# Performance work log

Measured on AMD Instinct MI355X. Metric: run time of the kernel, lower is better.

Reference implementation:

```python
import jax, jax.numpy as jnp
import numpy as np

B, T, D = 4, 1024, 1024
H = 16
DH = D // H  # 64
NEG = jnp.float32(-2.0**32 + 1)


def _sinusoid_table(T, D):
    pos = np.arange(T)[:, None]
    i = np.arange(D)[None, :]
    angle = pos / np.power(10000.0, 2.0 * (i // 2) / D)
    tab = np.zeros((T, D))
    tab[:, 0::2] = np.sin(angle[:, 0::2])
    tab[:, 1::2] = np.cos(angle[:, 1::2])
    return jnp.asarray(tab, dtype=jnp.float32)


def setup_inputs() -> dict:
    key = jax.random.key(0)
    ks = jax.random.split(key, 10)
    inp = {
        "queries": jax.random.normal(ks[0], (B, T, D), dtype=jnp.float32),
        "keys": jax.random.normal(ks[1], (B, T, D), dtype=jnp.float32),
        "query_lens": jax.random.randint(ks[2], (B, 1), 1, T + 1),
        "key_lens": jax.random.randint(ks[3], (B, 1), 1, T + 1),
        # learned params
        "pe_q": _sinusoid_table(T, D),
        "pe_k": _sinusoid_table(T, D),
        "W_Query": jax.random.truncated_normal(ks[4], -2.0, 2.0, (D, D), dtype=jnp.float32) * 0.05,
        "W_key": jax.random.truncated_normal(ks[5], -2.0, 2.0, (D, D), dtype=jnp.float32) * 0.05,
        "W_Value": jax.random.truncated_normal(ks[6], -2.0, 2.0, (D, D), dtype=jnp.float32) * 0.05,
        "fw1": jax.random.normal(ks[7], (D, 4 * D), dtype=jnp.float32) * (1.0 / np.sqrt(D)),
        "fw2": jax.random.normal(ks[8], (4 * D, D), dtype=jnp.float32) * (1.0 / np.sqrt(4 * D)),
    }
    return inp


def _forward(queries, keys, pe_q, pe_k, W_Query, W_key, W_Value, fw1, fw2,
             query_lens, key_lens):
    scale = jnp.float32(np.sqrt(D))
    # positional encoding (scale=True). NOTE: source bug preserved —
    # keys tensor is overwritten by key_pe applied to the PE'd queries.
    q_in = queries + pe_q[None] * scale          # [B,T,D]
    k_in = q_in + pe_k[None] * scale             # [B,T,D]

    Q = q_in @ W_Query                           # [B,T,D]
    K = k_in @ W_key                             # [B,T,D]
    V = K @ W_Value                              # NOTE: V projected from projected keys (source quirk)

    def heads(x):  # [B,T,D] -> [H,B,T,DH]
        return x.reshape(B, T, H, DH).transpose(2, 0, 1, 3)

    Qh, Kh, Vh = heads(Q), heads(K), heads(V)
    scores = jnp.einsum("hbqd,hbkd->hbqk", Qh, Kh) / jnp.float32(np.sqrt(DH))

    t = jnp.arange(T)
    kmask = (t[None, :] < key_lens).astype(jnp.float32)    # [B,T]
    qmask = (t[None, :] < query_lens).astype(jnp.float32)  # [B,T]

    scores = jnp.where(kmask[None, :, None, :] == 1.0, scores, NEG)
    # blinding: set diagonal to large negative
    eye = jnp.eye(T, dtype=bool)
    scores = jnp.where(eye[None, None], NEG, scores)

    scores = scores - scores.max(axis=-1, keepdims=True)
    probs = jax.nn.softmax(scores, axis=-1)
    probs = probs * qmask[None, :, :, None]

    out = jnp.einsum("hbqk,hbkd->hbqd", probs, Vh)         # [H,B,T,DH]
    result = out.transpose(1, 2, 0, 3).reshape(B, T, D)
    result = result + q_in                                  # residual uses PE'd queries

    ff = jnp.maximum(result @ fw1, 0.0) @ fw2
    result = result + ff
    return result.mean(axis=1, keepdims=True)               # [B,1,D]


def reference(queries, keys, query_lens, key_lens, pe_q, pe_k,
              W_Query, W_key, W_Value, fw1, fw2):
    return _forward(queries, keys, pe_q, pe_k, W_Query, W_key, W_Value,
                    fw1, fw2, query_lens, key_lens)
```

## Files before the change

### kernel.cpp

```cpp
#include <hip/hip_runtime.h>

#define T_ 1024
#define D_ 1024
#define B_ 4
#define H_ 16
#define DH_ 64
#define M_ (B_*T_)
#define NEG_ (-4294967295.0f)

typedef __attribute__((ext_vector_type(8))) _Float16 f16x8;
typedef __attribute__((ext_vector_type(4))) float f32x4;

__device__ __forceinline__ unsigned short f2h(float f) {
    _Float16 h = (_Float16)f; unsigned short u; __builtin_memcpy(&u, &h, 2); return u;
}
__device__ __forceinline__ float h2f(unsigned short u) {
    _Float16 h; __builtin_memcpy(&h, &u, 2); return (float)h;
}

typedef const unsigned int __attribute__((address_space(1)))* gas_p;
typedef unsigned int __attribute__((address_space(3)))* las_p;
__device__ __forceinline__ void gl_lds16(const void* g, void* l) {
    __builtin_amdgcn_global_load_lds((gas_p)g, (las_p)l, 16, 0, 0);
}

__global__ __launch_bounds__(256) void conv_a(const float* __restrict__ q,
                                              const float* __restrict__ peq,
                                              const float* __restrict__ pek,
                                              unsigned short* __restrict__ A2)
{
    int i = blockIdx.x * 256 + threadIdx.x;
    int m = i >> 8, c4 = (i & 255) << 2;
    ushort4 h;
    int mq = m & 4095;
    float4 qv = *(const float4*)(q + (size_t)mq * D_ + c4);
    float4 p  = *(const float4*)(peq + (size_t)(m & (T_-1)) * D_ + c4);
    if (m < 4096) {
        h.x = f2h(qv.x + 32.f*p.x); h.y = f2h(qv.y + 32.f*p.y);
        h.z = f2h(qv.z + 32.f*p.z); h.w = f2h(qv.w + 32.f*p.w);
    } else {
        float4 pk = *(const float4*)(pek + (size_t)(m & (T_-1)) * D_ + c4);
        h.x = f2h(qv.x + 32.f*(p.x + pk.x)); h.y = f2h(qv.y + 32.f*(p.y + pk.y));
        h.z = f2h(qv.z + 32.f*(p.z + pk.z)); h.w = f2h(qv.w + 32.f*(p.w + pk.w));
    }
    *(ushort4*)(A2 + (size_t)m * 1024 + c4) = h;
}

__global__ __launch_bounds__(256) void conv_w2(const float* __restrict__ Wq,
                                               const float* __restrict__ Wk,
                                               unsigned short* __restrict__ B2)
{
    __shared__ float t[32][33];
    const float* W = blockIdx.z ? Wk : Wq;
    int k0 = blockIdx.y * 32, n0 = blockIdx.x * 32;
    int r = threadIdx.x >> 5, c = threadIdx.x & 31;
    #pragma unroll
    for (int rr = 0; rr < 4; ++rr)
        t[r + 8*rr][c] = W[(size_t)(k0 + r + 8*rr) * 1024 + n0 + c];
    __syncthreads();
    #pragma unroll
    for (int rr = 0; rr < 4; ++rr)
        B2[(size_t)(blockIdx.z * 1024 + n0 + r + 8*rr) * 1024 + k0 + c] = f2h(t[c][r + 8*rr]);
}

__global__ __launch_bounds__(256) void conv_wT(const float* __restrict__ W,
                                               unsigned short* __restrict__ WT,
                                               int K, int N)
{
    __shared__ float t[32][33];
    int k0 = blockIdx.y * 32, n0 = blockIdx.x * 32;
    int r = threadIdx.x >> 5, c = threadIdx.x & 31;
    #pragma unroll
    for (int rr = 0; rr < 4; ++rr)
        t[r + 8*rr][c] = W[(size_t)(k0 + r + 8*rr) * N + n0 + c];
    __syncthreads();
    #pragma unroll
    for (int rr = 0; rr < 4; ++rr)
        WT[(size_t)(n0 + r + 8*rr) * K + k0 + c] = f2h(t[c][r + 8*rr]);
}

template<int BM>
__global__ __launch_bounds__(256) void gemm_mfma(
    const unsigned short* __restrict__ A, int lda,
    const unsigned short* __restrict__ B, int ldb, int K,
    float* __restrict__ outf,
    unsigned short* __restrict__ outh, unsigned short* __restrict__ outh2,
    int N, int flags,
    const int* __restrict__ qlv, const int* __restrict__ klv,
    float* __restrict__ hpart)
{
    constexpr int WN = (BM == 128) ? 2 : 4;
    constexpr int FN = 8 / WN;
    constexpr int NA = BM / 32;
    __shared__ __align__(16) unsigned short As[2][BM * 64];
    __shared__ __align__(16) unsigned short Bs[2][128 * 64];
    __shared__ float hp[4][64];
    const int tid = threadIdx.x;
    const int m0 = blockIdx.y * BM, n0 = blockIdx.x << 7;
    if (flags & 32) {
        if (m0 < 4096) {
            if (n0 >= 1024) return;
            if ((m0 & 1023) >= qlv[m0 >> 10]) return;
        } else {
            if (n0 < 1024) return;
            if ((m0 & 1023) >= klv[(m0 - 4096) >> 10]) return;
        }
    }
    if (flags & 256) {
        int bb = m0 >> 10, kl = klv[bb];
        if (kl > 1 && (m0 & 1023) >= kl) return;
    }
    const int lane = tid & 63, wave = tid >> 6;
    const int wm = (wave / WN) * 64;
    const int wn = (wave % WN) * (128 / WN);
    const int rl = lane & 15, kg = lane >> 4;
    const int rl7 = lane & 7;

    int ca[NA]; const unsigned short* gA[NA];
    #pragma unroll
    for (int i = 0; i < NA; ++i) {
        int c = i * 256 + tid;
        int row = c >> 3, k8 = (c & 7) ^ (row & 7);
        ca[i] = c * 8;
        gA[i] = A + (size_t)(m0 + row) * lda + k8 * 8;
    }
    int cb[4]; const unsigned short* gB[4];
    #pragma unroll
    for (int i = 0; i < 4; ++i) {
        int c = i * 256 + tid;
        int row = c >> 3, k8 = (c & 7) ^ (row & 7);
        cb[i] = c * 8;
        gB[i] = B + (size_t)(n0 + row) * ldb + k8 * 8;
    }

    int aoff[2][4], boff[2][FN];
    #pragma unroll
    for (int tt = 0; tt < 2; ++tt) {
        #pragma unroll
        for (int f = 0; f < 4; ++f)
            aoff[tt][f] = (wm + (f << 4) + rl) * 64 + (((tt * 4 + kg) ^ rl7) << 3);
        #pragma unroll
        for (int f = 0; f < FN; ++f)
            boff[tt][f] = (wn + (f << 4) + rl) * 64 + (((tt * 4 + kg) ^ rl7) << 3);
    }

    f32x4 acc[4][FN];
    #pragma unroll
    for (int i = 0; i < 4; ++i)
        #pragma unroll
        for (int j = 0; j < FN; ++j) {
            acc[i][j][0] = 0.f; acc[i][j][1] = 0.f;
            acc[i][j][2] = 0.f; acc[i][j][3] = 0.f;
        }

    const int NT = K >> 6;
    #pragma unroll
    for (int i = 0; i < 4; ++i)  gl_lds16(gB[i], &Bs[0][cb[i]]);
    #pragma unroll
    for (int i = 0; i < NA; ++i) gl_lds16(gA[i], &As[0][ca[i]]);
    #pragma unroll
    for (int i = 0; i < 4; ++i)  gl_lds16(gB[i] + 64, &Bs[1][cb[i]]);
    #pragma unroll
    for (int i = 0; i < NA; ++i) gl_lds16(gA[i] + 64, &As[1][ca[i]]);

    for (int t = 0; t < NT; ++t) {
        const int cur = t & 1;
        if (t + 1 < NT) {
            if constexpr (BM == 128) asm volatile("s_waitcnt vmcnt(8)" ::: "memory");
            else                     asm volatile("s_waitcnt vmcnt(6)" ::: "memory");
        } else {
            asm volatile("s_waitcnt vmcnt(0)" ::: "memory");
        }
        __builtin_amdgcn_s_barrier();
        __builtin_amdgcn_sched_barrier(0);
        f16x8 av[2][4], bv[2][FN];
        #pragma unroll
        for (int tt = 0; tt < 2; ++tt) {
            #pragma unroll
            for (int f = 0; f < 4; ++f)
                av[tt][f] = *(const f16x8*)&As[cur][aoff[tt][f]];
            #pragma unroll
            for (int f = 0; f < FN; ++f)
                bv[tt][f] = *(const f16x8*)&Bs[cur][boff[tt][f]];
        }
        asm volatile("s_waitcnt lgkmcnt(0)" ::: "memory");
        __builtin_amdgcn_sched_barrier(0);
        __builtin_amdgcn_s_barrier();
        __builtin_amdgcn_sched_barrier(0);
        if (t + 2 < NT) {
            const int ko = (t + 2) << 6;
            #pragma unroll
            for (int i = 0; i < 4; ++i)  gl_lds16(gB[i] + ko, &Bs[cur][cb[i]]);
            #pragma unroll
            for (int i = 0; i < NA; ++i) gl_lds16(gA[i] + ko, &As[cur][ca[i]]);
        }
        #pragma unroll
        for (int fm = 0; fm < 4; ++fm)
            #pragma unroll
            for (int fn = 0; fn < FN; ++fn) {
                acc[fm][fn] = __builtin_amdgcn_mfma_f32_16x16x32_f16(av[0][fm], bv[0][fn], acc[fm][fn], 0, 0, 0);
                acc[fm][fn] = __builtin_amdgcn_mfma_f32_16x16x32_f16(av[1][fm], bv[1][fn], acc[fm][fn], 0, 0, 0);
            }
    }

    if (flags & 128) {
        if constexpr (BM == 128) {
            #pragma unroll
            for (int fn = 0; fn < FN; ++fn) {
                float p = 0.f;
                #pragma unroll
                for (int fm = 0; fm < 4; ++fm)
                    #pragma unroll
                    for (int r = 0; r < 4; ++r) p += fmaxf(acc[fm][fn][r], 0.f);
                p += __shfl_xor(p, 16);
                p += __shfl_xor(p, 32);
                if (kg == 0) hp[wave][fn * 16 + rl] = p;
            }
            __syncthreads();
            if (tid < 128) {
                int c = tid;
                float s = (c < 64) ? (hp[0][c] + hp[2][c]) : (hp[1][c - 64] + hp[3][c - 64]);
                hpart[(size_t)blockIdx.y * 4096 + n0 + c] = s;
            }
        }
        return;
    }

    #pragma unroll
    for (int fm = 0; fm < 4; ++fm) {
        int row = m0 + wm + (fm << 4) + (kg << 2);
        #pragma unroll
        for (int fn = 0; fn < FN; ++fn) {
            int col = n0 + wn + (fn << 4) + rl;
            if (flags & 64) {
                ushort4 u;
                u.x = f2h(acc[fm][fn][0]); u.y = f2h(acc[fm][fn][1]);
                u.z = f2h(acc[fm][fn][2]); u.w = f2h(acc[fm][fn][3]);
                size_t a = ((size_t)((row >> 10) * 16 + (col >> 6)) * 64 + (col & 63)) * 1024 + (row & 1023);
                *(ushort4*)(outh + a) = u;
                continue;
            }
            #pragma unroll
            for (int r = 0; r < 4; ++r) {
                float x = acc[fm][fn][r];
                int rr = row + r;
                if (flags & 32) {
                    if (rr < 4096) outh[(size_t)rr * 1024 + col] = f2h(x);
                    else           outh2[(size_t)(rr - 4096) * 1024 + (col - 1024)] = f2h(x);
                } else {
                    size_t idx = (size_t)rr * N + col;
                    if (flags & 1)  x = fmaxf(x, 0.f);
                    if (flags & 8)  outf[idx] = x;
                    if (flags & 16) outh[idx] = f2h(x);
                }
            }
        }
    }
}

__global__ __launch_bounds__(256) void attn_mfma(
    const unsigned short* __restrict__ Qh,
    const unsigned short* __restrict__ Kh,
    const unsigned short* __restrict__ Vt,
    unsigned short* __restrict__ q16,
    const int* __restrict__ qlens, const int* __restrict__ klens)
{
    __shared__ __align__(16) unsigned short KS[4096];
    __shared__ __align__(16) unsigned short VtS[4096];
    __shared__ __align__(16) unsigned short Pl[4][1152];

    const int tid = threadIdx.x;
    const int bh = blockIdx.x & 63;
    const int qt = blockIdx.x >> 6;
    const int b = bh >> 4, h = bh & 15;
    const int qbase = qt * 64;
    const int qlen = qlens[b], klen = klens[b];
    if (qbase >= qlen) return;

    const int lane = tid & 63, wq = tid >> 6;
    const int rl = lane & 15, kg = lane >> 4, rl7 = lane & 7;
    const int gq = qbase + wq * 16 + rl;

    f16x8 qb[2];
    {
        const unsigned short* p1 = Qh + (size_t)(b * 1024 + gq) * 1024 + h * 64 + kg * 8;
        qb[0] = *(const f16x8*)p1;  qb[1] = *(const f16x8*)(p1 + 32);
    }

    const unsigned short* gK[2]; const unsigned short* gV[2];
    int cs[2];
    #pragma unroll
    for (int i = 0; i < 2; ++i) {
        int c = i * 256 + tid;
        int row = c >> 3, ch = (c & 7) ^ (row & 7);
        cs[i] = c * 8;
        gK[i] = Kh + (size_t)(b * 1024 + row) * 1024 + h * 64 + ch * 8;
        gV[i] = Vt + (size_t)(bh * 64 + row) * 1024 + ch * 8;
    }

    int akoff[4][2];
    #pragma unroll
    for (int mf = 0; mf < 4; ++mf)
        #pragma unroll
        for (int kh = 0; kh < 2; ++kh)
            akoff[mf][kh] = (mf * 16 + rl) * 64 + (((kg + 4 * kh) ^ rl7) << 3);

    f32x4 o[4];
    #pragma unroll
    for (int i = 0; i < 4; ++i) { o[i][0]=0.f; o[i][1]=0.f; o[i][2]=0.f; o[i][3]=0.f; }
    float m_run = -3.0e38f, l_run = 0.f;
    const int nt = (klen == 1) ? (T_ / 64) : ((klen + 63) >> 6);

    for (int kb = 0; kb < nt; ++kb) {
        const int kbase = kb * 64;
        const size_t koff = (size_t)kbase * 1024;
        gl_lds16(gK[0] + koff, &KS[cs[0]]);
        gl_lds16(gK[1] + koff, &KS[cs[1]]);
        gl_lds16(gV[0] + kbase, &VtS[cs[0]]);
        gl_lds16(gV[1] + kbase, &VtS[cs[1]]);
        __syncthreads();

        float v[4][4];
        __builtin_amdgcn_s_setprio(1);
        #pragma unroll
        for (int mf = 0; mf < 4; ++mf) {
            f32x4 s; s[0]=0.f; s[1]=0.f; s[2]=0.f; s[3]=0.f;
            f16x8 a0 = *(const f16x8*)&KS[akoff[mf][0]];
            f16x8 a1 = *(const f16x8*)&KS[akoff[mf][1]];
            s = __builtin_amdgcn_mfma_f32_16x16x32_f16(a0, qb[0], s, 0, 0, 0);
            s = __builtin_amdgcn_mfma_f32_16x16x32_f16(a1, qb[1], s, 0, 0, 0);
            #pragma unroll
            for (int r = 0; r < 4; ++r) {
                int gk = kbase + mf * 16 + kg * 4 + r;
                float x = s[r] * 0.125f;
                if (gk >= klen || gk == gq) x = NEG_;
                v[mf][r] = x;
            }
        }
        __builtin_amdgcn_s_setprio(0);
        float mt = -3.0e38f;
        #pragma unroll
        for (int mf = 0; mf < 4; ++mf)
            #pragma unroll
            for (int r = 0; r < 4; ++r) mt = fmaxf(mt, v[mf][r]);
        mt = fmaxf(mt, __shfl_xor(mt, 16));
        mt = fmaxf(mt, __shfl_xor(mt, 32));
        float mnew = fmaxf(m_run, mt);
        float fac = __expf(m_run - mnew);
        float sum = 0.f;
        #pragma unroll
        for (int mf = 0; mf < 4; ++mf) {
            ushort4 pb;
            pb.x = f2h(__expf(v[mf][0] - mnew));
            pb.y = f2h(__expf(v[mf][1] - mnew));
            pb.z = f2h(__expf(v[mf][2] - mnew));
            pb.w = f2h(__expf(v[mf][3] - mnew));
            sum += h2f(pb.x) + h2f(pb.y) + h2f(pb.z) + h2f(pb.w);
            *(ushort4*)&Pl[wq][rl * 72 + mf * 16 + kg * 4] = pb;
        }
        sum += __shfl_xor(sum, 16);
        sum += __shfl_xor(sum, 32);
        l_run = l_run * fac + sum;
        m_run = mnew;
        #pragma unroll
        for (int i = 0; i < 4; ++i) {
            o[i][0] *= fac; o[i][1] *= fac; o[i][2] *= fac; o[i][3] *= fac;
        }
        f16x8 bp0 = *(const f16x8*)&Pl[wq][rl * 72 + kg * 8];
        f16x8 bp1 = *(const f16x8*)&Pl[wq][rl * 72 + 32 + kg * 8];
        __builtin_amdgcn_s_setprio(1);
        #pragma unroll
        for (int dmf = 0; dmf < 4; ++dmf) {
            f16x8 a0 = *(const f16x8*)&VtS[akoff[dmf][0]];
            f16x8 a1 = *(const f16x8*)&VtS[akoff[dmf][1]];
            o[dmf] = __builtin_amdgcn_mfma_f32_16x16x32_f16(a0, bp0, o[dmf], 0, 0, 0);
            o[dmf] = __builtin_amdgcn_mfma_f32_16x16x32_f16(a1, bp1, o[dmf], 0, 0, 0);
        }
        __builtin_amdgcn_s_setprio(0);
        __syncthreads();
    }

    float invl = (gq < qlen) ? (1.f / l_run) : 0.f;
    #pragma unroll
    for (int dmf = 0; dmf < 4; ++dmf)
        #pragma unroll
        for (int r = 0; r < 4; ++r) {
            int dh = dmf * 16 + kg * 4 + r;
            size_t a = (size_t)(b * 1024 + gq) * 1024 + h * 64 + dh;
            q16[a] = f2h(o[dmf][r] * invl + h2f(q16[a]));
        }
}

__global__ __launch_bounds__(256) void mean16(const unsigned short* __restrict__ X,
                                              float* __restrict__ out, int Xdim)
{
    __shared__ float red[4][128];
    int tid = threadIdx.x;
    int b = blockIdx.y;
    int dbase = blockIdx.x * 128;
    int tq = tid >> 6, dd = tid & 63;
    int d = dbase + dd * 2;
    const unsigned short* p = X + ((size_t)b * T_ + tq * 256) * Xdim + d;
    float s0 = 0.f, s1 = 0.f;
    for (int t = 0; t < 256; ++t) {
        ushort2 v = *(const ushort2*)(p + (size_t)t * Xdim);
        s0 += h2f(v.x); s1 += h2f(v.y);
    }
    red[tq][dd*2] = s0; red[tq][dd*2 + 1] = s1;
    __syncthreads();
    if (tq == 0) {
        float a = red[0][dd*2] + red[1][dd*2] + red[2][dd*2] + red[3][dd*2];
        float c = red[0][dd*2+1] + red[1][dd*2+1] + red[2][dd*2+1] + red[3][dd*2+1];
        out[(size_t)b * Xdim + d]     = a * (1.f/1024.f);
        out[(size_t)b * Xdim + d + 1] = c * (1.f/1024.f);
    }
}

__global__ __launch_bounds__(256) void final_partial(const float* __restrict__ Hpart,
                                                     const float* __restrict__ fw2,
                                                     float* __restrict__ Pout)
{
    __shared__ float red[4][4][64];
    __shared__ float hm[4][128];
    int tid = threadIdx.x;
    #pragma unroll
    for (int s = 0; s < 2; ++s) {
        int idx = s * 256 + tid;
        int bb = idx >> 7, jl = idx & 127;
        int j = blockIdx.y * 128 + jl;
        float acc = 0.f;
        #pragma unroll
        for (int i = 0; i < 8; ++i)
            acc += Hpart[((size_t)(bb * 8 + i)) * 4096 + j];
        hm[bb][jl] = acc * (1.f / 1024.f);
    }
    __syncthreads();
    int dd = tid & 63;
    int d = blockIdx.x * 64 + dd;
    int jq = tid >> 6;
    float s4[4] = {0.f, 0.f, 0.f, 0.f};
    for (int jj = 0; jj < 32; ++jj) {
        int jl = jq * 32 + jj;
        int j = blockIdx.y * 128 + jl;
        float wv = fw2[(size_t)j * 1024 + d];
        s4[0] += hm[0][jl] * wv;
        s4[1] += hm[1][jl] * wv;
        s4[2] += hm[2][jl] * wv;
        s4[3] += hm[3][jl] * wv;
    }
    #pragma unroll
    for (int bb = 0; bb < 4; ++bb) red[jq][bb][dd] = s4[bb];
    __syncthreads();
    if (jq == 0) {
        #pragma unroll
        for (int bb = 0; bb < 4; ++bb) {
            float tot = red[0][bb][dd] + red[1][bb][dd] + red[2][bb][dd] + red[3][bb][dd];
            Pout[((size_t)blockIdx.y * 4 + bb) * 1024 + d] = tot;
        }
    }
}

__global__ __launch_bounds__(256) void reduce_out(const float* __restrict__ Mres,
                                                  const float* __restrict__ Pout,
                                                  float* __restrict__ out)
{
    int idx = blockIdx.x * 256 + threadIdx.x;
    int b = idx >> 10, d = idx & 1023;
    float s = Mres[(size_t)b * 1024 + d];
    #pragma unroll
    for (int jy = 0; jy < 32; ++jy)
        s += Pout[((size_t)jy * 4 + b) * 1024 + d];
    out[(size_t)b * 1024 + d] = s;
}

extern "C" void kernel_launch(void* const* d_in, const int* in_sizes, int n_in,
                              void* d_out, int out_size, void* d_ws, size_t ws_size,
                              hipStream_t stream)
{
    const float* queries = (const float*)d_in[0];
    const int*   qlens   = (const int*)d_in[2];
    const int*   klens   = (const int*)d_in[3];
    const float* pe_q    = (const float*)d_in[4];
    const float* pe_k    = (const float*)d_in[5];
    const float* Wq      = (const float*)d_in[6];
    const float* Wk      = (const float*)d_in[7];
    const float* Wv      = (const float*)d_in[8];
    const float* fw1     = (const float*)d_in[9];
    const float* fw2     = (const float*)d_in[10];
    float* out = (float*)d_out;

    char* w = (char*)d_ws;
    unsigned short* Qh   = (unsigned short*)(w);
    unsigned short* A2   = (unsigned short*)(w + (8ll  << 20));
    unsigned short* q16  = A2;
    unsigned short* Kh16 = (unsigned short*)(w + (24ll << 20));
    unsigned short* B2   = (unsigned short*)(w + (32ll << 20));
    unsigned short* WvT  = (unsigned short*)(w + (36ll << 20));
    unsigned short* Vt   = (unsigned short*)(w + (38ll << 20));
    unsigned short* fw1T = (unsigned short*)(w + (46ll << 20));
    float*          Hpart= (float*)(w + (54ll << 20));
    float*          Mres = (float*)(w + (55ll << 20));
    float*          Pout = (float*)(w + (56ll << 20));

    conv_a <<<8192, 256, 0, stream>>>(queries, pe_q, pe_k, A2);
    conv_w2<<<dim3(32, 32, 2), 256, 0, stream>>>(Wq, Wk, B2);
    conv_wT<<<dim3(32, 32), 256, 0, stream>>>(Wv, WvT, 1024, 1024);
    conv_wT<<<dim3(128, 32), 256, 0, stream>>>(fw1, fw1T, 1024, 4096);
    gemm_mfma<128><<<dim3(16, 64), 256, 0, stream>>>(
        A2, 1024, B2, 1024, 1024,
        nullptr, Qh, Kh16, 2048, 32, qlens, klens, nullptr);
    gemm_mfma<64><<<dim3(8, 64), 256, 0, stream>>>(
        Kh16, 1024, WvT, 1024, 1024,
        nullptr, Vt, nullptr, 1024, 64 | 256, nullptr, klens, nullptr);
    attn_mfma<<<1024, 256, 0, stream>>>(Qh, Kh16, Vt, q16, qlens, klens);
    gemm_mfma<128><<<dim3(32, 32), 256, 0, stream>>>(
        q16, 1024, fw1T, 1024, 1024,
        nullptr, nullptr, nullptr, 4096, 128, nullptr, nullptr, Hpart);
    mean16<<<dim3(8, 4), 256, 0, stream>>>(q16, Mres, 1024);
    final_partial<<<dim3(16, 32), 256, 0, stream>>>(Hpart, fw2, Pout);
    reduce_out<<<16, 256, 0, stream>>>(Mres, Pout, out);
}
```

Baseline: 144.8 us.

## Merge conversion kernels into one launch and halve GEMM K-tile depth

The four input and weight conversion kernels are folded into a single launch that dispatches on block index, which removes three kernel launches and their tail gaps. The MFMA GEMM K-tile drops from 64 to 32, halving LDS buffer size (more blocks per CU possible) and changing the swizzle to 4-way, with the wait counts adjusted to match. In exchange there are twice as many loop iterations and barriers per tile, and less work per barrier to hide latency.

```diff
diff --git a/kernel.cpp b/kernel.cpp
--- a/kernel.cpp
+++ b/kernel.cpp
@@ -24,59 +24,71 @@
     __builtin_amdgcn_global_load_lds((gas_p)g, (las_p)l, 16, 0, 0);
 }
 
-__global__ __launch_bounds__(256) void conv_a(const float* __restrict__ q,
-                                              const float* __restrict__ peq,
-                                              const float* __restrict__ pek,
-                                              unsigned short* __restrict__ A2)
-{
-    int i = blockIdx.x * 256 + threadIdx.x;
-    int m = i >> 8, c4 = (i & 255) << 2;
-    ushort4 h;
-    int mq = m & 4095;
-    float4 qv = *(const float4*)(q + (size_t)mq * D_ + c4);
-    float4 p  = *(const float4*)(peq + (size_t)(m & (T_-1)) * D_ + c4);
-    if (m < 4096) {
-        h.x = f2h(qv.x + 32.f*p.x); h.y = f2h(qv.y + 32.f*p.y);
-        h.z = f2h(qv.z + 32.f*p.z); h.w = f2h(qv.w + 32.f*p.w);
+__global__ __launch_bounds__(256) void conv_all(const float* __restrict__ q,
+                                                const float* __restrict__ peq,
+                                                const float* __restrict__ pek,
+                                                const float* __restrict__ Wq,
+                                                const float* __restrict__ Wk,
+                                                const float* __restrict__ Wv,
+                                                const float* __restrict__ fw1,
+                                                unsigned short* __restrict__ A2,
+                                                unsigned short* __restrict__ B2,
+                                                unsigned short* __restrict__ WvT,
+                                                unsigned short* __restrict__ fw1T)
+{
+    int blk = blockIdx.x;
+    if (blk < 8192) {
+        int i = blk * 256 + threadIdx.x;
+        int m = i >> 8, c4 = (i & 255) << 2;
+        int mq = m & 4095;
+        float4 qv = *(const float4*)(q + (size_t)mq * D_ + c4);
+        float4 p  = *(const float4*)(peq + (size_t)(m & (T_-1)) * D_ + c4);
+        ushort4 h;
+        if (m < 4096) {
+            h.x = f2h(qv.x + 32.f*p.x); h.y = f2h(qv.y + 32.f*p.y);
+            h.z = f2h(qv.z + 32.f*p.z); h.w = f2h(qv.w + 32.f*p.w);
+        } else {
+            float4 pk = *(const float4*)(pek + (size_t)(m & (T_-1)) * D_ + c4);
+            h.x = f2h(qv.x + 32.f*(p.x + pk.x)); h.y = f2h(qv.y + 32.f*(p.y + pk.y));
+            h.z = f2h(qv.z + 32.f*(p.z + pk.z)); h.w = f2h(qv.w + 32.f*(p.w + pk.w));
+        }
+        *(ushort4*)(A2 + (size_t)m * 1024 + c4) = h;
+        return;
+    }
+    __shared__ float t[32][33];
+    int r = threadIdx.x >> 5, c = threadIdx.x & 31;
+    if (blk < 10240) {
+        int l = blk - 8192;
+        int z = l >> 10, k0 = ((l >> 5) & 31) * 32, n0 = (l & 31) * 32;
+        const float* W = z ? Wk : Wq;
+        #pragma unroll
+        for (int rr = 0; rr < 4; ++rr)
+            t[r + 8*rr][c] = W[(size_t)(k0 + r + 8*rr) * 1024 + n0 + c];
+        __syncthreads();
+        #pragma unroll
+        for (int rr = 0; rr < 4; ++rr)
+            B2[(size_t)(z * 1024 + n0 + r + 8*rr) * 1024 + k0 + c] = f2h(t[c][r + 8*rr]);
+    } else if (blk < 11264) {
+        int l = blk - 10240;
+        int k0 = (l >> 5) * 32, n0 = (l & 31) * 32;
+        #pragma unroll
+        for (int rr = 0; rr < 4; ++rr)
+            t[r + 8*rr][c] = Wv[(size_t)(k0 + r + 8*rr) * 1024 + n0 + c];
+        __syncthreads();
+        #pragma unroll
+        for (int rr = 0; rr < 4; ++rr)
+            WvT[(size_t)(n0 + r + 8*rr) * 1024 + k0 + c] = f2h(t[c][r + 8*rr]);
     } else {
-        float4 pk = *(const float4*)(pek + (size_t)(m & (T_-1)) * D_ + c4);
-        h.x = f2h(qv.x + 32.f*(p.x + pk.x)); h.y = f2h(qv.y + 32.f*(p.y + pk.y));
-        h.z = f2h(qv.z + 32.f*(p.z + pk.z)); h.w = f2h(qv.w + 32.f*(p.w + pk.w));
-    }
-    *(ushort4*)(A2 + (size_t)m * 1024 + c4) = h;
-}
-
-__global__ __launch_bounds__(256) void conv_w2(const float* __restrict__ Wq,
-                                               const float* __restrict__ Wk,
-                                               unsigned short* __restrict__ B2)
-{
-    __shared__ float t[32][33];
-    const float* W = blockIdx.z ? Wk : Wq;
-    int k0 = blockIdx.y * 32, n0 = blockIdx.x * 32;
-    int r = threadIdx.x >> 5, c = threadIdx.x & 31;
-    #pragma unroll
-    for (int rr = 0; rr < 4; ++rr)
-        t[r + 8*rr][c] = W[(size_t)(k0 + r + 8*rr) * 1024 + n0 + c];
-    __syncthreads();
-    #pragma unroll
-    for (int rr = 0; rr < 4; ++rr)
-        B2[(size_t)(blockIdx.z * 1024 + n0 + r + 8*rr) * 1024 + k0 + c] = f2h(t[c][r + 8*rr]);
-}
-
-__global__ __launch_bounds__(256) void conv_wT(const float* __restrict__ W,
-                                               unsigned short* __restrict__ WT,
-                                               int K, int N)
-{
-    __shared__ float t[32][33];
-    int k0 = blockIdx.y * 32, n0 = blockIdx.x * 32;
-    int r = threadIdx.x >> 5, c = threadIdx.x & 31;
-    #pragma unroll
-    for (int rr = 0; rr < 4; ++rr)
-        t[r + 8*rr][c] = W[(size_t)(k0 + r + 8*rr) * N + n0 + c];
-    __syncthreads();
-    #pragma unroll
-    for (int rr = 0; rr < 4; ++rr)
-        WT[(size_t)(n0 + r + 8*rr) * K + k0 + c] = f2h(t[c][r + 8*rr]);
+        int l = blk - 11264;
+        int k0 = (l >> 7) * 32, n0 = (l & 127) * 32;
+        #pragma unroll
+        for (int rr = 0; rr < 4; ++rr)
+            t[r + 8*rr][c] = fw1[(size_t)(k0 + r + 8*rr) * 4096 + n0 + c];
+        __syncthreads();
+        #pragma unroll
+        for (int rr = 0; rr < 4; ++rr)
+            fw1T[(size_t)(n0 + r + 8*rr) * 1024 + k0 + c] = f2h(t[c][r + 8*rr]);
+    }
 }
 
 template<int BM>
@@ -91,9 +103,9 @@
 {
     constexpr int WN = (BM == 128) ? 2 : 4;
     constexpr int FN = 8 / WN;
-    constexpr int NA = BM / 32;
-    __shared__ __align__(16) unsigned short As[2][BM * 64];
-    __shared__ __align__(16) unsigned short Bs[2][128 * 64];
+    constexpr int NA = BM / 64;
+    __shared__ __align__(16) unsigned short As[2][BM * 32];
+    __shared__ __align__(16) unsigned short Bs[2][128 * 32];
     __shared__ float hp[4][64];
     const int tid = threadIdx.x;
     const int m0 = blockIdx.y * BM, n0 = blockIdx.x << 7;
@@ -114,35 +126,32 @@
     const int wm = (wave / WN) * 64;
     const int wn = (wave % WN) * (128 / WN);
     const int rl = lane & 15, kg = lane >> 4;
-    const int rl7 = lane & 7;
+    const int rl3 = lane & 3;
 
     int ca[NA]; const unsigned short* gA[NA];
     #pragma unroll
     for (int i = 0; i < NA; ++i) {
         int c = i * 256 + tid;
-        int row = c >> 3, k8 = (c & 7) ^ (row & 7);
+        int row = c >> 2, k8 = (c & 3) ^ (row & 3);
         ca[i] = c * 8;
         gA[i] = A + (size_t)(m0 + row) * lda + k8 * 8;
     }
-    int cb[4]; const unsigned short* gB[4];
-    #pragma unroll
-    for (int i = 0; i < 4; ++i) {
+    int cb[2]; const unsigned short* gB[2];
+    #pragma unroll
+    for (int i = 0; i < 2; ++i) {
         int c = i * 256 + tid;
-        int row = c >> 3, k8 = (c & 7) ^ (row & 7);
+        int row = c >> 2, k8 = (c & 3) ^ (row & 3);
         cb[i] = c * 8;
         gB[i] = B + (size_t)(n0 + row) * ldb + k8 * 8;
     }
 
-    int aoff[2][4], boff[2][FN];
-    #pragma unroll
-    for (int tt = 0; tt < 2; ++tt) {
-        #pragma unroll
-        for (int f = 0; f < 4; ++f)
-            aoff[tt][f] = (wm + (f << 4) + rl) * 64 + (((tt * 4 + kg) ^ rl7) << 3);
-        #pragma unroll
-        for (int f = 0; f < FN; ++f)
-            boff[tt][f] = (wn + (f << 4) + rl) * 64 + (((tt * 4 + kg) ^ rl7) << 3);
-    }
+    int aoff[4], boff[FN];
+    #pragma unroll
+    for (int f = 0; f < 4; ++f)
+        aoff[f] = (wm + (f << 4) + rl) * 32 + ((kg ^ rl3) << 3);
+    #pragma unroll
+    for (int f = 0; f < FN; ++f)
+        boff[f] = (wn + (f << 4) + rl) * 32 + ((kg ^ rl3) << 3);
 
     f32x4 acc[4][FN];
     #pragma unroll
@@ -153,54 +162,49 @@
             acc[i][j][2] = 0.f; acc[i][j][3] = 0.f;
         }
 
-    const int NT = K >> 6;
-    #pragma unroll
-    for (int i = 0; i < 4; ++i)  gl_lds16(gB[i], &Bs[0][cb[i]]);
+    const int NT = K >> 5;
+    #pragma unroll
+    for (int i = 0; i < 2; ++i)  gl_lds16(gB[i], &Bs[0][cb[i]]);
     #pragma unroll
     for (int i = 0; i < NA; ++i) gl_lds16(gA[i], &As[0][ca[i]]);
     #pragma unroll
-    for (int i = 0; i < 4; ++i)  gl_lds16(gB[i] + 64, &Bs[1][cb[i]]);
-    #pragma unroll
-    for (int i = 0; i < NA; ++i) gl_lds16(gA[i] + 64, &As[1][ca[i]]);
+    for (int i = 0; i < 2; ++i)  gl_lds16(gB[i] + 32, &Bs[1][cb[i]]);
+    #pragma unroll
+    for (int i = 0; i < NA; ++i) gl_lds16(gA[i] + 32, &As[1][ca[i]]);
 
     for (int t = 0; t < NT; ++t) {
         const int cur = t & 1;
         if (t + 1 < NT) {
-            if constexpr (BM == 128) asm volatile("s_waitcnt vmcnt(8)" ::: "memory");
-            else                     asm volatile("s_waitcnt vmcnt(6)" ::: "memory");
+            if constexpr (BM == 128) asm volatile("s_waitcnt vmcnt(4)" ::: "memory");
+            else                     asm volatile("s_waitcnt vmcnt(3)" ::: "memory");
         } else {
             asm volatile("s_waitcnt vmcnt(0)" ::: "memory");
         }
         __builtin_amdgcn_s_barrier();
         __builtin_amdgcn_sched_barrier(0);
-        f16x8 av[2][4], bv[2][FN];
-        #pragma unroll
-        for (int tt = 0; tt < 2; ++tt) {
-            #pragma unroll
-            for (int f = 0; f < 4; ++f)
-                av[tt][f] = *(const f16x8*)&As[cur][aoff[tt][f]];
-            #pragma unroll
-            for (int f = 0; f < FN; ++f)
-                bv[tt][f] = *(const f16x8*)&Bs[cur][boff[tt][f]];
-        }
+        f16x8 av[4], bv[FN];
+        #pragma unroll
+        for (int f = 0; f < 4; ++f)
+            av[f] = *(const f16x8*)&As[cur][aoff[f]];
+        #pragma unroll
+        for (int f = 0; f < FN; ++f)
+            bv[f] = *(const f16x8*)&Bs[cur][boff[f]];
         asm volatile("s_waitcnt lgkmcnt(0)" ::: "memory");
         __builtin_amdgcn_sched_barrier(0);
         __builtin_amdgcn_s_barrier();
         __builtin_amdgcn_sched_barrier(0);
         if (t + 2 < NT) {
-            const int ko = (t + 2) << 6;
-            #pragma unroll
-            for (int i = 0; i < 4; ++i)  gl_lds16(gB[i] + ko, &Bs[cur][cb[i]]);
+            const int ko = (t + 2) << 5;
+            #pragma unroll
+            for (int i = 0; i < 2; ++i)  gl_lds16(gB[i] + ko, &Bs[cur][cb[i]]);
             #pragma unroll
             for (int i = 0; i < NA; ++i) gl_lds16(gA[i] + ko, &As[cur][ca[i]]);
         }
         #pragma unroll
         for (int fm = 0; fm < 4; ++fm)
             #pragma unroll
-            for (int fn = 0; fn < FN; ++fn) {
-                acc[fm][fn] = __builtin_amdgcn_mfma_f32_16x16x32_f16(av[0][fm], bv[0][fn], acc[fm][fn], 0, 0, 0);
-                acc[fm][fn] = __builtin_amdgcn_mfma_f32_16x16x32_f16(av[1][fm], bv[1][fn], acc[fm][fn], 0, 0, 0);
-            }
+            for (int fn = 0; fn < FN; ++fn)
+                acc[fm][fn] = __builtin_amdgcn_mfma_f32_16x16x32_f16(av[fm], bv[fn], acc[fm][fn], 0, 0, 0);
     }
 
     if (flags & 128) {
@@ -502,10 +506,8 @@
     float*          Mres = (float*)(w + (55ll << 20));
     float*          Pout = (float*)(w + (56ll << 20));
 
-    conv_a <<<8192, 256, 0, stream>>>(queries, pe_q, pe_k, A2);
-    conv_w2<<<dim3(32, 32, 2), 256, 0, stream>>>(Wq, Wk, B2);
-    conv_wT<<<dim3(32, 32), 256, 0, stream>>>(Wv, WvT, 1024, 1024);
-    conv_wT<<<dim3(128, 32), 256, 0, stream>>>(fw1, fw1T, 1024, 4096);
+    conv_all<<<15360, 256, 0, stream>>>(queries, pe_q, pe_k, Wq, Wk, Wv, fw1,
+                                        A2, B2, WvT, fw1T);
     gemm_mfma<128><<<dim3(16, 64), 256, 0, stream>>>(
         A2, 1024, B2, 1024, 1024,
         nullptr, Qh, Kh16, 2048, 32, qlens, klens, nullptr);
```

Result: slower. 157.7 us (+8.9%).
